# Performance work log

Hardware: AMD Instinct MI355X
Metric: run time of the kernel (lower is better)

The kernel has to match this reference:

```python
import jax, jax.numpy as jnp
import numpy as np

N_EMBED = 384
N_HEAD = 6
HEAD_DIM = N_EMBED // N_HEAD


def setup_inputs() -> dict:
    key = jax.random.key(0)
    k1, k2, k3 = jax.random.split(key, 3)
    B, T = 128, 256
    x = jax.random.normal(k1, (B, T, N_EMBED), dtype=jnp.float32)
    # nn.Linear(N_EMBED, 3*N_EMBED, bias=False): weight [3*N_EMBED, N_EMBED],
    # applied as x @ W.T -> store transposed [N_EMBED, 3*N_EMBED]
    W_qkv = jax.random.normal(k2, (N_EMBED, 3 * N_EMBED), dtype=jnp.float32) * (N_EMBED ** -0.5)
    W_proj = jax.random.normal(k3, (N_EMBED, N_EMBED), dtype=jnp.float32) * (N_EMBED ** -0.5)
    return {"x": x, "W_qkv": W_qkv, "W_proj": W_proj}


def reference(x, W_qkv, W_proj):
    B, T, C = x.shape
    qkv = jnp.einsum('btc,cd->btd', x, W_qkv)  # [B,T,3C]
    q, k, v = jnp.split(qkv, 3, axis=-1)
    # [B, H, T, Dh]
    q = q.reshape(B, T, N_HEAD, HEAD_DIM).transpose(0, 2, 1, 3)
    k = k.reshape(B, T, N_HEAD, HEAD_DIM).transpose(0, 2, 1, 3)
    v = v.reshape(B, T, N_HEAD, HEAD_DIM).transpose(0, 2, 1, 3)
    scale = HEAD_DIM ** -0.5
    wei = jnp.einsum('bhqd,bhkd->bhqk', q, k) * scale  # [B,H,T,T]
    causal = jnp.tril(jnp.ones((T, T), dtype=bool))
    wei = jnp.where(causal[None, None, :, :], wei, -jnp.inf)
    wei = jax.nn.softmax(wei, axis=-1)
    # dropout layers are identity in eval mode
    out = jnp.einsum('bhqk,bhkd->bhqd', wei, v)  # [B,H,T,Dh]
    out = out.transpose(0, 2, 1, 3).reshape(B, T, C)
    out = jnp.einsum('btc,cd->btd', out, W_proj)
    return out
```

## Files before the change

kernel.cpp:

```cpp
#include <hip/hip_runtime.h>
#include <hip/hip_bf16.h>

typedef __attribute__((ext_vector_type(8))) short short8;
typedef __attribute__((ext_vector_type(4))) float f32x4;

typedef const __attribute__((address_space(1))) void* gas_p;
typedef __attribute__((address_space(3))) void* las_p;
#define GLOAD_LDS16(g, l) __builtin_amdgcn_global_load_lds((gas_p)(const void*)(g), (las_p)(void*)(l), 16, 0, 0)

__device__ __forceinline__ unsigned short f2bf(float f) {
    union { float f; unsigned int u; } v; v.f = f;
    unsigned int r = v.u + 0x7FFFu + ((v.u >> 16) & 1u);
    return (unsigned short)(r >> 16);
}

__global__ __launch_bounds__(256) void cast_x_kernel(
    const float* __restrict__ x, unsigned short* __restrict__ xb, int n8)
{
    int i = blockIdx.x * 256 + threadIdx.x;
    if (i >= n8) return;
    const float4* p = (const float4*)x + (size_t)i * 2;
    float4 a = p[0], b = p[1];
    short8 o;
    o[0] = (short)f2bf(a.x); o[1] = (short)f2bf(a.y);
    o[2] = (short)f2bf(a.z); o[3] = (short)f2bf(a.w);
    o[4] = (short)f2bf(b.x); o[5] = (short)f2bf(b.y);
    o[6] = (short)f2bf(b.z); o[7] = (short)f2bf(b.w);
    *(short8*)(xb + (size_t)i * 8) = o;
}

__global__ __launch_bounds__(256) void cast_wt_kernel(
    const float* __restrict__ W, unsigned short* __restrict__ Wt, int K, int N)
{
    int idx = blockIdx.x * 256 + threadIdx.x;
    if (idx >= N * K) return;
    int n = idx / K, k = idx - n * K;
    Wt[idx] = f2bf(W[(size_t)k * N + n]);
}

template<int MODE>
__global__ __launch_bounds__(256, 2) void gemm_bt_kernel(
    const unsigned short* __restrict__ A, const unsigned short* __restrict__ Bt,
    void* __restrict__ C0, unsigned short* __restrict__ C1,
    int M, int N, int K)
{
    __shared__ __align__(16) unsigned short As[128 * 64];
    __shared__ __align__(16) unsigned short Bs[128 * 64];
    const int tid = threadIdx.x;
    const int lane = tid & 63, wv = tid >> 6;
    const int c = lane & 15, g = lane >> 4;
    const int wm = (wv >> 1) * 64, wn = (wv & 1) * 64;
    const long m0 = (long)blockIdx.x * 128, n0 = (long)blockIdx.y * 128;

    f32x4 acc[4][4] = {};

    for (int kt = 0; kt < K; kt += 64) {
        #pragma unroll
        for (int i = 0; i < 4; ++i) {
            int ch = i * 256 + wv * 64 + lane;
            int row = ch >> 3, col = (ch & 7) * 8;
            const unsigned short* ga = &A[(m0 + row) * (size_t)K + kt + col];
            const unsigned short* gb = &Bt[(n0 + row) * (size_t)K + kt + col];
            unsigned short* la = &As[(i * 256 + wv * 64) * 8];
            unsigned short* lb = &Bs[(i * 256 + wv * 64) * 8];
            GLOAD_LDS16(ga, la);
            GLOAD_LDS16(gb, lb);
        }
        __syncthreads();
        #pragma unroll
        for (int ks = 0; ks < 2; ++ks) {
            short8 af[4], bf_[4];
            #pragma unroll
            for (int i = 0; i < 4; ++i)
                af[i] = *(const short8*)&As[(wm + i * 16 + c) * 64 + ks * 32 + g * 8];
            #pragma unroll
            for (int i = 0; i < 4; ++i)
                bf_[i] = *(const short8*)&Bs[(wn + i * 16 + c) * 64 + ks * 32 + g * 8];
            #pragma unroll
            for (int mi = 0; mi < 4; ++mi)
                #pragma unroll
                for (int ni = 0; ni < 4; ++ni)
                    acc[mi][ni] = __builtin_amdgcn_mfma_f32_16x16x32_bf16(
                        af[mi], bf_[ni], acc[mi][ni], 0, 0, 0);
        }
        __syncthreads();
    }

    if (MODE == 1) {
        #pragma unroll
        for (int mi = 0; mi < 4; ++mi)
            #pragma unroll
            for (int ni = 0; ni < 4; ++ni)
                #pragma unroll
                for (int r = 0; r < 4; ++r) {
                    long m = m0 + wm + mi * 16 + g * 4 + r;
                    long n = n0 + wn + ni * 16 + c;
                    ((float*)C0)[m * N + n] = acc[mi][ni][r];
                }
    } else if (n0 < 768) {
        #pragma unroll
        for (int mi = 0; mi < 4; ++mi)
            #pragma unroll
            for (int ni = 0; ni < 4; ++ni)
                #pragma unroll
                for (int r = 0; r < 4; ++r) {
                    long m = m0 + wm + mi * 16 + g * 4 + r;
                    long n = n0 + wn + ni * 16 + c;
                    ((unsigned short*)C0)[m * 768 + n] = f2bf(acc[mi][ni][r]);
                }
    } else {
        char* wbase = (char*)As + wv * 8192;
        #pragma unroll
        for (int ni = 0; ni < 4; ++ni)
            #pragma unroll
            for (int mi = 0; mi < 4; ++mi)
                #pragma unroll
                for (int r = 0; r < 4; ++r) {
                    int d = ni * 16 + c, t = mi * 16 + g * 4 + r;
                    int byte = (d * 128 + t * 2) ^ ((d & 7) << 4);
                    *(unsigned short*)(wbase + byte) = f2bf(acc[mi][ni][r]);
                }
        __asm__ __volatile__("" ::: "memory");
        int h = (int)((n0 + wn - 768) >> 6);
        long b = (m0 + wm) >> 8;
        int t0 = (int)((m0 + wm) & 255);
        long bh = b * 6 + h;
        #pragma unroll
        for (int it = 0; it < 8; ++it) {
            int d = it * 8 + (lane >> 3), ck = lane & 7;
            short8 v = *(const short8*)(wbase + ((d * 128 + ck * 16) ^ ((d & 7) << 4)));
            *(short8*)&C1[(bh * 64 + d) * 256 + t0 + ck * 8] = v;
        }
    }
}

__global__ __launch_bounds__(256, 2) void attn_kernel(
    const unsigned short* __restrict__ qk,
    const unsigned short* __restrict__ vt,
    unsigned short* __restrict__ outp)
{
    const int bh = blockIdx.x;
    const int b = bh / 6, h = bh - b * 6;
    const int tid = threadIdx.x;
    const int lane = tid & 63, wv = tid >> 6;
    const int c = lane & 15, g = lane >> 4;

    __shared__ unsigned short Ks[256 * 64];
    __shared__ unsigned short Vs[64 * 256];
    __shared__ unsigned short Pl[4][32 * 64];

    #pragma unroll
    for (int it = 0; it < 8; ++it) {
        int ch = it * 256 + tid;
        {
            int row = ch >> 3, col = (ch & 7) * 8;
            int db = (row * 128 + col * 2) ^ ((row & 7) << 4);
            *(short8*)((char*)Ks + db) =
                *(const short8*)&qk[(size_t)(b * 256 + row) * 768 + 384 + h * 64 + col];
        }
        {
            int d = ch >> 5, tk = (ch & 31) * 8;
            int db = (d * 512 + tk * 2) ^ ((d & 7) << 4);
            *(short8*)((char*)Vs + db) =
                *(const short8*)&vt[((size_t)bh * 64 + d) * 256 + tk];
        }
    }

    const int ptile[2] = { wv, 7 - wv };
    short8 aq[2][2][2];
    #pragma unroll
    for (int t = 0; t < 2; ++t)
        #pragma unroll
        for (int mi = 0; mi < 2; ++mi)
            #pragma unroll
            for (int ks = 0; ks < 2; ++ks)
                aq[t][mi][ks] = *(const short8*)&qk[
                    (size_t)(b * 256 + ptile[t] * 32 + mi * 16 + c) * 768 + h * 64 + ks * 32 + g * 8];

    __syncthreads();

    f32x4 o[2][2][4] = {};
    float mrun[2][2][4], lrun[2][2][4];
    #pragma unroll
    for (int t = 0; t < 2; ++t)
        #pragma unroll
        for (int mi = 0; mi < 2; ++mi)
            #pragma unroll
            for (int r = 0; r < 4; ++r) { mrun[t][mi][r] = -1e30f; lrun[t][mi][r] = 0.f; }

    #pragma unroll
    for (int t = 0; t < 2; ++t) {
        const int p = ptile[t];
        const int jlast = p >> 1;
        const int modd = (p & 1) * 32;
        for (int j = 0; j <= jlast; ++j) {
            short8 bk[4][2];
            #pragma unroll
            for (int ni = 0; ni < 4; ++ni)
                #pragma unroll
                for (int ks = 0; ks < 2; ++ks) {
                    int key = j * 64 + ni * 16 + c;
                    bk[ni][ks] = *(const short8*)((char*)Ks +
                        ((key * 128 + (ks * 32 + g * 8) * 2) ^ ((key & 7) << 4)));
                }
            #pragma unroll
            for (int mi = 0; mi < 2; ++mi) {
                f32x4 s[4];
                #pragma unroll
                for (int ni = 0; ni < 4; ++ni) {
                    f32x4 z = {0.f, 0.f, 0.f, 0.f};
                    z = __builtin_amdgcn_mfma_f32_16x16x32_bf16(aq[t][mi][0], bk[ni][0], z, 0, 0, 0);
                    z = __builtin_amdgcn_mfma_f32_16x16x32_bf16(aq[t][mi][1], bk[ni][1], z, 0, 0, 0);
                    s[ni] = z;
                }
                float pv[4][4];
                #pragma unroll
                for (int ni = 0; ni < 4; ++ni)
                    #pragma unroll
                    for (int r = 0; r < 4; ++r) {
                        float v = s[ni][r] * 0.125f;
                        if (j == jlast) {
                            int kloc = ni * 16 + c, qloc = mi * 16 + g * 4 + r;
                            if (kloc > qloc + modd) v = -1e30f;
                        }
                        pv[ni][r] = v;
                    }
                #pragma unroll
                for (int r = 0; r < 4; ++r) {
                    float m1 = fmaxf(fmaxf(pv[0][r], pv[1][r]), fmaxf(pv[2][r], pv[3][r]));
                    #pragma unroll
                    for (int off = 8; off >= 1; off >>= 1)
                        m1 = fmaxf(m1, __shfl_xor(m1, off, 16));
                    float mold = mrun[t][mi][r];
                    float mnew = fmaxf(mold, m1);
                    float fac = __expf(mold - mnew);
                    float ssum = 0.f;
                    #pragma unroll
                    for (int ni = 0; ni < 4; ++ni) {
                        float pp = __expf(pv[ni][r] - mnew);
                        pv[ni][r] = pp;
                        ssum += pp;
                    }
                    #pragma unroll
                    for (int off = 8; off >= 1; off >>= 1)
                        ssum += __shfl_xor(ssum, off, 16);
                    lrun[t][mi][r] = lrun[t][mi][r] * fac + ssum;
                    mrun[t][mi][r] = mnew;
                    #pragma unroll
                    for (int nd = 0; nd < 4; ++nd) o[t][mi][nd][r] *= fac;
                }
                #pragma unroll
                for (int ni = 0; ni < 4; ++ni)
                    #pragma unroll
                    for (int r = 0; r < 4; ++r) {
                        int rl = mi * 16 + g * 4 + r;
                        int pb = (rl * 128 + (ni * 16 + c) * 2) ^ ((rl & 7) << 4);
                        *(unsigned short*)((char*)Pl[wv] + pb) = f2bf(pv[ni][r]);
                    }
            }
            __asm__ __volatile__("" ::: "memory");

            short8 bv_[4][2];
            #pragma unroll
            for (int nd = 0; nd < 4; ++nd)
                #pragma unroll
                for (int ks = 0; ks < 2; ++ks) {
                    int d = nd * 16 + c;
                    bv_[nd][ks] = *(const short8*)((char*)Vs +
                        ((d * 512 + (j * 64 + ks * 32 + g * 8) * 2) ^ ((d & 7) << 4)));
                }
            #pragma unroll
            for (int mi = 0; mi < 2; ++mi) {
                short8 ap[2];
                #pragma unroll
                for (int ks = 0; ks < 2; ++ks)
                    ap[ks] = *(const short8*)((char*)Pl[wv] +
                        (((mi * 16 + c) * 128 + (ks * 32 + g * 8) * 2) ^ ((c & 7) << 4)));
                #pragma unroll
                for (int nd = 0; nd < 4; ++nd) {
                    o[t][mi][nd] = __builtin_amdgcn_mfma_f32_16x16x32_bf16(ap[0], bv_[nd][0], o[t][mi][nd], 0, 0, 0);
                    o[t][mi][nd] = __builtin_amdgcn_mfma_f32_16x16x32_bf16(ap[1], bv_[nd][1], o[t][mi][nd], 0, 0, 0);
                }
            }
            __asm__ __volatile__("" ::: "memory");
        }
    }

    #pragma unroll
    for (int t = 0; t < 2; ++t)
        #pragma unroll
        for (int mi = 0; mi < 2; ++mi) {
            float inv[4];
            #pragma unroll
            for (int r = 0; r < 4; ++r) inv[r] = 1.0f / lrun[t][mi][r];
            #pragma unroll
            for (int nd = 0; nd < 4; ++nd)
                #pragma unroll
                for (int r = 0; r < 4; ++r) {
                    int q = ptile[t] * 32 + mi * 16 + g * 4 + r;
                    int dd = h * 64 + nd * 16 + c;
                    outp[((size_t)b * 256 + q) * 384 + dd] = f2bf(o[t][mi][nd][r] * inv[r]);
                }
        }
}

extern "C" void kernel_launch(void* const* d_in, const int* in_sizes, int n_in,
                              void* d_out, int out_size, void* d_ws, size_t ws_size,
                              hipStream_t stream) {
    const float* x     = (const float*)d_in[0];
    const float* Wqkv  = (const float*)d_in[1];
    const float* Wproj = (const float*)d_in[2];

    char* ws = (char*)d_ws;
    unsigned short* xb     = (unsigned short*)(ws);
    unsigned short* wqkvt  = (unsigned short*)(ws + 25165824);
    unsigned short* wprojt = (unsigned short*)(ws + 26050560);
    unsigned short* qkb    = (unsigned short*)(ws + 26345472);
    unsigned short* vtb    = (unsigned short*)(ws + 76677120);
    unsigned short* attnb  = (unsigned short*)(ws + 101842944);

    cast_x_kernel<<<6144, 256, 0, stream>>>(x, xb, 1572864);
    cast_wt_kernel<<<1728, 256, 0, stream>>>(Wqkv, wqkvt, 384, 1152);
    cast_wt_kernel<<<576, 256, 0, stream>>>(Wproj, wprojt, 384, 384);

    gemm_bt_kernel<0><<<dim3(256, 9), 256, 0, stream>>>(xb, wqkvt, (void*)qkb, vtb, 32768, 1152, 384);
    attn_kernel<<<768, 256, 0, stream>>>(qkb, vtb, attnb);
    gemm_bt_kernel<1><<<dim3(256, 3), 256, 0, stream>>>(attnb, wprojt, d_out, nullptr, 32768, 384, 384);
}
```

Baseline: 120.6 us.

## Restructure attention kernel with transposed MFMA, V read from global, and higher occupancy

The attention kernel now computes S transposed (K as the A operand), so each lane owns one query column. Softmax reductions need only two cross-group shuffles instead of per-row 16-lane shuffles, and the output is written as packed 4-element vectors. V is no longer staged in LDS; it is loaded from global memory each key tile. The per-wave P buffer shrinks and the two query tiles are processed one after the other instead of holding both sets of accumulators at once. Together these cut LDS use and registers so launch bounds can ask for three blocks per CU. The cost is repeated global V loads that depend on L2 hits, and more work in serial order per wave.

```diff
diff --git a/kernel.cpp b/kernel.cpp
--- a/kernel.cpp
+++ b/kernel.cpp
@@ -3,6 +3,7 @@
 
 typedef __attribute__((ext_vector_type(8))) short short8;
 typedef __attribute__((ext_vector_type(4))) float f32x4;
+typedef __attribute__((ext_vector_type(4))) unsigned short ush4;
 
 typedef const __attribute__((address_space(1))) void* gas_p;
 typedef __attribute__((address_space(3))) void* las_p;
@@ -12,6 +13,9 @@
     union { float f; unsigned int u; } v; v.f = f;
     unsigned int r = v.u + 0x7FFFu + ((v.u >> 16) & 1u);
     return (unsigned short)(r >> 16);
+}
+__device__ __forceinline__ unsigned pk2(float a, float b) {
+    return (unsigned)f2bf(a) | ((unsigned)f2bf(b) << 16);
 }
 
 __global__ __launch_bounds__(256) void cast_x_kernel(
@@ -134,7 +138,7 @@
     }
 }
 
-__global__ __launch_bounds__(256, 2) void attn_kernel(
+__global__ __launch_bounds__(256, 3) void attn_kernel(
     const unsigned short* __restrict__ qk,
     const unsigned short* __restrict__ vt,
     unsigned short* __restrict__ outp)
@@ -146,54 +150,46 @@
     const int c = lane & 15, g = lane >> 4;
 
     __shared__ unsigned short Ks[256 * 64];
-    __shared__ unsigned short Vs[64 * 256];
-    __shared__ unsigned short Pl[4][32 * 64];
+    __shared__ unsigned short Pl[4][16 * 64];
 
     #pragma unroll
     for (int it = 0; it < 8; ++it) {
         int ch = it * 256 + tid;
-        {
-            int row = ch >> 3, col = (ch & 7) * 8;
-            int db = (row * 128 + col * 2) ^ ((row & 7) << 4);
-            *(short8*)((char*)Ks + db) =
-                *(const short8*)&qk[(size_t)(b * 256 + row) * 768 + 384 + h * 64 + col];
-        }
-        {
-            int d = ch >> 5, tk = (ch & 31) * 8;
-            int db = (d * 512 + tk * 2) ^ ((d & 7) << 4);
-            *(short8*)((char*)Vs + db) =
-                *(const short8*)&vt[((size_t)bh * 64 + d) * 256 + tk];
-        }
+        int row = ch >> 3, col = (ch & 7) * 8;
+        int db = (row * 128 + col * 2) ^ ((row & 7) << 4);
+        *(short8*)((char*)Ks + db) =
+            *(const short8*)&qk[(size_t)(b * 256 + row) * 768 + 384 + h * 64 + col];
     }
-
-    const int ptile[2] = { wv, 7 - wv };
-    short8 aq[2][2][2];
-    #pragma unroll
-    for (int t = 0; t < 2; ++t)
-        #pragma unroll
-        for (int mi = 0; mi < 2; ++mi)
-            #pragma unroll
-            for (int ks = 0; ks < 2; ++ks)
-                aq[t][mi][ks] = *(const short8*)&qk[
-                    (size_t)(b * 256 + ptile[t] * 32 + mi * 16 + c) * 768 + h * 64 + ks * 32 + g * 8];
-
     __syncthreads();
 
-    f32x4 o[2][2][4] = {};
-    float mrun[2][2][4], lrun[2][2][4];
-    #pragma unroll
-    for (int t = 0; t < 2; ++t)
-        #pragma unroll
-        for (int mi = 0; mi < 2; ++mi)
-            #pragma unroll
-            for (int r = 0; r < 4; ++r) { mrun[t][mi][r] = -1e30f; lrun[t][mi][r] = 0.f; }
-
-    #pragma unroll
+    char* plw = (char*)Pl[wv];
+
     for (int t = 0; t < 2; ++t) {
-        const int p = ptile[t];
+        const int p = t ? 7 - wv : wv;
         const int jlast = p >> 1;
         const int modd = (p & 1) * 32;
+        const int qt0 = p * 32;
+
+        short8 aq[2][2];
+        #pragma unroll
+        for (int mi = 0; mi < 2; ++mi)
+            #pragma unroll
+            for (int ks = 0; ks < 2; ++ks)
+                aq[mi][ks] = *(const short8*)&qk[
+                    (size_t)(b * 256 + qt0 + mi * 16 + c) * 768 + h * 64 + ks * 32 + g * 8];
+
+        f32x4 o[2][4] = {};
+        float mrun[2] = {-1e30f, -1e30f}, lrun[2] = {0.f, 0.f};
+
         for (int j = 0; j <= jlast; ++j) {
+            short8 bv[4][2];
+            #pragma unroll
+            for (int nd = 0; nd < 4; ++nd)
+                #pragma unroll
+                for (int ks = 0; ks < 2; ++ks)
+                    bv[nd][ks] = *(const short8*)&vt[
+                        ((size_t)bh * 64 + nd * 16 + c) * 256 + j * 64 + ks * 32 + g * 8];
+
             short8 bk[4][2];
             #pragma unroll
             for (int ni = 0; ni < 4; ++ni)
@@ -203,105 +199,91 @@
                     bk[ni][ks] = *(const short8*)((char*)Ks +
                         ((key * 128 + (ks * 32 + g * 8) * 2) ^ ((key & 7) << 4)));
                 }
+
             #pragma unroll
             for (int mi = 0; mi < 2; ++mi) {
-                f32x4 s[4];
+                float pv[4][4];
                 #pragma unroll
                 for (int ni = 0; ni < 4; ++ni) {
                     f32x4 z = {0.f, 0.f, 0.f, 0.f};
-                    z = __builtin_amdgcn_mfma_f32_16x16x32_bf16(aq[t][mi][0], bk[ni][0], z, 0, 0, 0);
-                    z = __builtin_amdgcn_mfma_f32_16x16x32_bf16(aq[t][mi][1], bk[ni][1], z, 0, 0, 0);
-                    s[ni] = z;
-                }
-                float pv[4][4];
+                    z = __builtin_amdgcn_mfma_f32_16x16x32_bf16(bk[ni][0], aq[mi][0], z, 0, 0, 0);
+                    z = __builtin_amdgcn_mfma_f32_16x16x32_bf16(bk[ni][1], aq[mi][1], z, 0, 0, 0);
+                    #pragma unroll
+                    for (int r = 0; r < 4; ++r) {
+                        float v = z[r] * 0.125f;
+                        if (j == jlast) {
+                            int kloc = ni * 16 + g * 4 + r;
+                            int qloc = mi * 16 + c + modd;
+                            if (kloc > qloc) v = -1e30f;
+                        }
+                        pv[ni][r] = v;
+                    }
+                }
+                float m01 = fmaxf(fmaxf(pv[0][0], pv[0][1]), fmaxf(pv[0][2], pv[0][3]));
+                float m11 = fmaxf(fmaxf(pv[1][0], pv[1][1]), fmaxf(pv[1][2], pv[1][3]));
+                float m21 = fmaxf(fmaxf(pv[2][0], pv[2][1]), fmaxf(pv[2][2], pv[2][3]));
+                float m31 = fmaxf(fmaxf(pv[3][0], pv[3][1]), fmaxf(pv[3][2], pv[3][3]));
+                float m1 = fmaxf(fmaxf(m01, m11), fmaxf(m21, m31));
+                m1 = fmaxf(m1, __shfl_xor(m1, 16));
+                m1 = fmaxf(m1, __shfl_xor(m1, 32));
+                float mold = mrun[mi];
+                float mnew = fmaxf(mold, m1);
+                float fac = __expf(mold - mnew);
+                float ssum = 0.f;
                 #pragma unroll
                 for (int ni = 0; ni < 4; ++ni)
                     #pragma unroll
                     for (int r = 0; r < 4; ++r) {
-                        float v = s[ni][r] * 0.125f;
-                        if (j == jlast) {
-                            int kloc = ni * 16 + c, qloc = mi * 16 + g * 4 + r;
-                            if (kloc > qloc + modd) v = -1e30f;
-                        }
-                        pv[ni][r] = v;
-                    }
-                #pragma unroll
-                for (int r = 0; r < 4; ++r) {
-                    float m1 = fmaxf(fmaxf(pv[0][r], pv[1][r]), fmaxf(pv[2][r], pv[3][r]));
-                    #pragma unroll
-                    for (int off = 8; off >= 1; off >>= 1)
-                        m1 = fmaxf(m1, __shfl_xor(m1, off, 16));
-                    float mold = mrun[t][mi][r];
-                    float mnew = fmaxf(mold, m1);
-                    float fac = __expf(mold - mnew);
-                    float ssum = 0.f;
-                    #pragma unroll
-                    for (int ni = 0; ni < 4; ++ni) {
                         float pp = __expf(pv[ni][r] - mnew);
                         pv[ni][r] = pp;
                         ssum += pp;
                     }
+                ssum += __shfl_xor(ssum, 16);
+                ssum += __shfl_xor(ssum, 32);
+                lrun[mi] = lrun[mi] * fac + ssum;
+                mrun[mi] = mnew;
+                #pragma unroll
+                for (int nd = 0; nd < 4; ++nd)
                     #pragma unroll
-                    for (int off = 8; off >= 1; off >>= 1)
-                        ssum += __shfl_xor(ssum, off, 16);
-                    lrun[t][mi][r] = lrun[t][mi][r] * fac + ssum;
-                    mrun[t][mi][r] = mnew;
-                    #pragma unroll
-                    for (int nd = 0; nd < 4; ++nd) o[t][mi][nd][r] *= fac;
-                }
-                #pragma unroll
-                for (int ni = 0; ni < 4; ++ni)
-                    #pragma unroll
-                    for (int r = 0; r < 4; ++r) {
-                        int rl = mi * 16 + g * 4 + r;
-                        int pb = (rl * 128 + (ni * 16 + c) * 2) ^ ((rl & 7) << 4);
-                        *(unsigned short*)((char*)Pl[wv] + pb) = f2bf(pv[ni][r]);
-                    }
+                    for (int r = 0; r < 4; ++r) o[mi][nd][r] *= fac;
+
+                __asm__ __volatile__("" ::: "memory");
+                #pragma unroll
+                for (int ni = 0; ni < 4; ++ni) {
+                    uint2 w;
+                    w.x = pk2(pv[ni][0], pv[ni][1]);
+                    w.y = pk2(pv[ni][2], pv[ni][3]);
+                    *(uint2*)(plw + ((c * 128 + ni * 32 + g * 8) ^ ((c & 7) << 4))) = w;
+                }
+                __asm__ __volatile__("" ::: "memory");
+
+                short8 ap[2];
+                #pragma unroll
+                for (int ks = 0; ks < 2; ++ks)
+                    ap[ks] = *(const short8*)(plw +
+                        ((c * 128 + ks * 64 + g * 16) ^ ((c & 7) << 4)));
+
+                #pragma unroll
+                for (int nd = 0; nd < 4; ++nd) {
+                    o[mi][nd] = __builtin_amdgcn_mfma_f32_16x16x32_bf16(bv[nd][0], ap[0], o[mi][nd], 0, 0, 0);
+                    o[mi][nd] = __builtin_amdgcn_mfma_f32_16x16x32_bf16(bv[nd][1], ap[1], o[mi][nd], 0, 0, 0);
+                }
+                __asm__ __volatile__("" ::: "memory");
             }
-            __asm__ __volatile__("" ::: "memory");
-
-            short8 bv_[4][2];
-            #pragma unroll
-            for (int nd = 0; nd < 4; ++nd)
-                #pragma unroll
-                for (int ks = 0; ks < 2; ++ks) {
-                    int d = nd * 16 + c;
-                    bv_[nd][ks] = *(const short8*)((char*)Vs +
-                        ((d * 512 + (j * 64 + ks * 32 + g * 8) * 2) ^ ((d & 7) << 4)));
-                }
-            #pragma unroll
-            for (int mi = 0; mi < 2; ++mi) {
-                short8 ap[2];
-                #pragma unroll
-                for (int ks = 0; ks < 2; ++ks)
-                    ap[ks] = *(const short8*)((char*)Pl[wv] +
-                        (((mi * 16 + c) * 128 + (ks * 32 + g * 8) * 2) ^ ((c & 7) << 4)));
-                #pragma unroll
-                for (int nd = 0; nd < 4; ++nd) {
-                    o[t][mi][nd] = __builtin_amdgcn_mfma_f32_16x16x32_bf16(ap[0], bv_[nd][0], o[t][mi][nd], 0, 0, 0);
-                    o[t][mi][nd] = __builtin_amdgcn_mfma_f32_16x16x32_bf16(ap[1], bv_[nd][1], o[t][mi][nd], 0, 0, 0);
-                }
+        }
+
+        #pragma unroll
+        for (int mi = 0; mi < 2; ++mi) {
+            float inv = 1.0f / lrun[mi];
+            #pragma unroll
+            for (int nd = 0; nd < 4; ++nd) {
+                ush4 w;
+                #pragma unroll
+                for (int r = 0; r < 4; ++r) w[r] = f2bf(o[mi][nd][r] * inv);
+                *(ush4*)&outp[((size_t)b * 256 + qt0 + mi * 16 + c) * 384 + h * 64 + nd * 16 + g * 4] = w;
             }
-            __asm__ __volatile__("" ::: "memory");
         }
     }
-
-    #pragma unroll
-    for (int t = 0; t < 2; ++t)
-        #pragma unroll
-        for (int mi = 0; mi < 2; ++mi) {
-            float inv[4];
-            #pragma unroll
-            for (int r = 0; r < 4; ++r) inv[r] = 1.0f / lrun[t][mi][r];
-            #pragma unroll
-            for (int nd = 0; nd < 4; ++nd)
-                #pragma unroll
-                for (int r = 0; r < 4; ++r) {
-                    int q = ptile[t] * 32 + mi * 16 + g * 4 + r;
-                    int dd = h * 64 + nd * 16 + c;
-                    outp[((size_t)b * 256 + q) * 384 + dd] = f2bf(o[t][mi][nd][r] * inv[r]);
-                }
-        }
 }
 
 extern "C" void kernel_launch(void* const* d_in, const int* in_sizes, int n_in,
```

After: 116.4 us. 3.5% less time.
